# Optimization experiments

Measured on AMD Instinct MI355X. Metric: run time of the kernel, lower is better.

## Reference

```python
import math
import jax, jax.numpy as jnp
import numpy as np

B, T, D = 1, 4096, 1024
NH, NKV, HD = 16, 4, 64          # nhead, n_kv_heads, head_dim
WINDOW = 256


def _alibi_slopes(nhead: int) -> np.ndarray:
    closest_pow2 = 2 ** math.floor(math.log2(nhead))
    base = 2.0 ** (-2.0 ** (-(math.log2(closest_pow2) - 3)))
    slopes = base ** np.arange(1, closest_pow2 + 1, dtype=np.float32)
    if closest_pow2 < nhead:
        extra_base = 2.0 ** (-2.0 ** (-(math.log2(2 * closest_pow2) - 3)))
        extra = extra_base ** np.arange(1, 2 * (nhead - closest_pow2) + 1, 2, dtype=np.float32)
        slopes = np.concatenate([slopes, extra])
    return slopes.astype(np.float32)


def setup_inputs() -> dict:
    key = jax.random.key(0)
    ks = jax.random.split(key, 9)
    s = 0.02
    return {
        "x": jax.random.normal(ks[0], (B, T, D), jnp.float32),
        "Wq": jax.random.normal(ks[1], (D, NH * HD), jnp.float32) * s,
        "bq": jax.random.normal(ks[2], (NH * HD,), jnp.float32) * s,
        "Wk": jax.random.normal(ks[3], (D, NKV * HD), jnp.float32) * s,
        "bk": jax.random.normal(ks[4], (NKV * HD,), jnp.float32) * s,
        "Wv": jax.random.normal(ks[5], (D, NKV * HD), jnp.float32) * s,
        "bv": jax.random.normal(ks[6], (NKV * HD,), jnp.float32) * s,
        "Wo": jax.random.normal(ks[7], (D, D), jnp.float32) * s,
        "bo": jax.random.normal(ks[8], (D,), jnp.float32) * s,
    }


def _attn_bias():
    # ALiBi bias + causal + sliding-window mask, shape (NH, T, T)
    pos = jnp.arange(T)
    dist = pos[None, :] - pos[:, None]          # col - row; <=0 where causal-allowed
    allowed = (dist <= 0) & (-dist < WINDOW)    # causal AND within window
    slopes = jnp.asarray(_alibi_slopes(NH))     # (NH,)
    bias = -slopes[:, None, None] * jnp.abs(dist)[None].astype(jnp.float32)
    return jnp.where(allowed[None], bias, -jnp.inf)  # (NH, T, T)


def reference(x, Wq, bq, Wk, bk, Wv, bv, Wo, bo):
    q = (x @ Wq + bq).reshape(B, T, NH, HD).transpose(0, 2, 1, 3)   # (B,NH,T,HD)
    k = (x @ Wk + bk).reshape(B, T, NKV, HD).transpose(0, 2, 1, 3)  # (B,NKV,T,HD)
    v = (x @ Wv + bv).reshape(B, T, NKV, HD).transpose(0, 2, 1, 3)
    # GQA: repeat_interleave kv heads to NH
    k = jnp.repeat(k, NH // NKV, axis=1)
    v = jnp.repeat(v, NH // NKV, axis=1)
    scale = 1.0 / math.sqrt(HD)
    scores = jnp.einsum("bhtd,bhsd->bhts", q, k) * scale + _attn_bias()[None]
    probs = jax.nn.softmax(scores, axis=-1)
    out = jnp.einsum("bhts,bhsd->bhtd", probs, v)        # (B,NH,T,HD)
    out = out.transpose(0, 2, 1, 3).reshape(B, T, D)
    return out @ Wo + bo
```

## Files before the change

### kernel.cpp

```cpp
#include <hip/hip_runtime.h>

typedef __bf16 bf16;
typedef __bf16 bf16x8 __attribute__((ext_vector_type(8)));
typedef float f32x4 __attribute__((ext_vector_type(4)));

#define T_LEN   4096
#define D_MODEL 1024
#define QKV_LD  1536
#define VT_LD   4128
#define WINDOW  256

__device__ __forceinline__ void gload_lds16(const bf16* g, bf16* l) {
    __builtin_amdgcn_global_load_lds((const __attribute__((address_space(1))) void*)g,
                                     (__attribute__((address_space(3))) void*)l, 16, 0, 0);
}


__global__ void cvt_f32_bf16(const float* __restrict__ in, bf16* __restrict__ out, int n) {
    int i = (blockIdx.x * blockDim.x + threadIdx.x) * 8;
    if (i >= n) return;
    float4 a = *(const float4*)(in + i);
    float4 b = *(const float4*)(in + i + 4);
    bf16x8 o;
    o[0] = (bf16)a.x; o[1] = (bf16)a.y; o[2] = (bf16)a.z; o[3] = (bf16)a.w;
    o[4] = (bf16)b.x; o[5] = (bf16)b.y; o[6] = (bf16)b.z; o[7] = (bf16)b.w;
    *(bf16x8*)(out + i) = o;
}

__global__ void transpose_wqkv(const float* __restrict__ Wq, const float* __restrict__ Wk,
                               const float* __restrict__ Wv, bf16* __restrict__ Wt) {
    __shared__ float t[32][33];
    int n0 = blockIdx.x * 32, k0 = blockIdx.y * 32;
    const float* W; int Ns, nofs;
    if (n0 < 1024)      { W = Wq; Ns = 1024; nofs = 0; }
    else if (n0 < 1280) { W = Wk; Ns = 256;  nofs = 1024; }
    else                { W = Wv; Ns = 256;  nofs = 1280; }
    int tx = threadIdx.x & 31, ty = threadIdx.x >> 5;
#pragma unroll
    for (int it = 0; it < 4; ++it)
        t[ty + it * 8][tx] = W[(size_t)(k0 + ty + it * 8) * Ns + (n0 - nofs) + tx];
    __syncthreads();
#pragma unroll
    for (int it = 0; it < 4; ++it)
        Wt[(size_t)(n0 + ty + it * 8) * 1024 + k0 + tx] = (bf16)t[tx][ty + it * 8];
}

__global__ void transpose_w(const float* __restrict__ W, bf16* __restrict__ Wt, int K, int N) {
    __shared__ float t[32][33];
    int n0 = blockIdx.x * 32, k0 = blockIdx.y * 32;
    int tx = threadIdx.x & 31, ty = threadIdx.x >> 5;
#pragma unroll
    for (int it = 0; it < 4; ++it)
        t[ty + it * 8][tx] = W[(size_t)(k0 + ty + it * 8) * N + n0 + tx];
    __syncthreads();
#pragma unroll
    for (int it = 0; it < 4; ++it)
        Wt[(size_t)(n0 + ty + it * 8) * K + k0 + tx] = (bf16)t[tx][ty + it * 8];
}

__global__ void transpose_v(const bf16* __restrict__ QKV, bf16* __restrict__ Vt) {
    __shared__ bf16 t[32][33];
    int t0 = blockIdx.x * 32;
    int c0 = blockIdx.y * 32;
    int tx = threadIdx.x & 31, ty = threadIdx.x >> 5;
#pragma unroll
    for (int it = 0; it < 4; ++it)
        t[ty + it * 8][tx] = QKV[(size_t)(t0 + ty + it * 8) * QKV_LD + 1280 + c0 + tx];
    __syncthreads();
#pragma unroll
    for (int it = 0; it < 4; ++it)
        Vt[(size_t)(c0 + ty + it * 8) * VT_LD + t0 + tx] = t[tx][ty + it * 8];
}


template <bool OUT_BF16, bool QKV_BIAS>
__global__ __launch_bounds__(256) void gemm_bt(
    const bf16* __restrict__ A, const bf16* __restrict__ Bt,
    const float* __restrict__ b0, const float* __restrict__ b1,
    const float* __restrict__ b2, void* __restrict__ Cv,
    int M, int N, int K)
{
    __shared__ bf16 As[128 * 32];
    __shared__ bf16 Bs[64 * 32];
    const int m0 = blockIdx.y * 128;
    const int n0 = blockIdx.x * 64;
    const int tid  = threadIdx.x;
    const int wave = tid >> 6, lane = tid & 63;
    const int quad = lane >> 4, l16 = lane & 15;
    const int wm = wave >> 1, wn = wave & 1;

    f32x4 acc[4][2] = {};

    const int srow = wave * 16 + (lane >> 2);
    const int scol = (lane & 3) * 8;
    const bf16* ga0 = A  + (size_t)(m0 + srow) * K + scol;
    const bf16* ga1 = A  + (size_t)(m0 + srow + 64) * K + scol;
    const bf16* gb  = Bt + (size_t)(n0 + srow) * K + scol;
    bf16* la0 = As + srow * 32 + scol;
    bf16* la1 = As + (srow + 64) * 32 + scol;
    bf16* lb  = Bs + srow * 32 + scol;

    const int nk = K >> 5;
    for (int kt = 0; kt < nk; ++kt) {
        __syncthreads();
        gload_lds16(ga0 + kt * 32, la0);
        gload_lds16(ga1 + kt * 32, la1);
        gload_lds16(gb  + kt * 32, lb);
        __syncthreads();
        bf16x8 af[4], bfr[2];
#pragma unroll
        for (int i = 0; i < 4; ++i)
            af[i] = *(const bf16x8*)&As[(wm * 64 + i * 16 + l16) * 32 + quad * 8];
#pragma unroll
        for (int j = 0; j < 2; ++j)
            bfr[j] = *(const bf16x8*)&Bs[(wn * 32 + j * 16 + l16) * 32 + quad * 8];
#pragma unroll
        for (int i = 0; i < 4; ++i)
#pragma unroll
            for (int j = 0; j < 2; ++j)
                acc[i][j] = __builtin_amdgcn_mfma_f32_16x16x32_bf16(af[i], bfr[j], acc[i][j], 0, 0, 0);
    }

#pragma unroll
    for (int i = 0; i < 4; ++i)
#pragma unroll
        for (int j = 0; j < 2; ++j) {
            const int col = n0 + wn * 32 + j * 16 + l16;
            const float bb = QKV_BIAS
                ? (col < 1024 ? b0[col] : (col < 1280 ? b1[col - 1024] : b2[col - 1280]))
                : b0[col];
#pragma unroll
            for (int r = 0; r < 4; ++r) {
                const int row = m0 + wm * 64 + i * 16 + quad * 4 + r;
                const float v = acc[i][j][r] + bb;
                if (OUT_BF16) ((bf16*)Cv)[(size_t)row * N + col] = (bf16)v;
                else          ((float*)Cv)[(size_t)row * N + col] = v;
            }
        }
}


__global__ __launch_bounds__(256) void attn_kernel(
    const bf16* __restrict__ QKV, const bf16* __restrict__ Vt, bf16* __restrict__ Oa)
{
    __shared__ bf16 Ps[4][16][296];
    const int wave = threadIdx.x >> 6;
    const int lane = threadIdx.x & 63;
    const int q0 = (blockIdx.x * 4 + wave) * 16;
    const int h  = blockIdx.y;
    const int kh = h >> 2;
    const int quad = lane >> 4, l16 = lane & 15;
    const float slope = exp2f(-0.5f * (float)(h + 1));
    const int lo = (q0 >= 256) ? (q0 - 256) : 0;

    const bf16* qp = QKV + (size_t)(q0 + l16) * QKV_LD + h * 64 + quad * 8;
    bf16x8 qf0 = *(const bf16x8*)qp;
    bf16x8 qf1 = *(const bf16x8*)(qp + 32);

    f32x4 s[17];
#pragma unroll
    for (int t = 0; t < 17; ++t) {
        const bf16* kp = QKV + (size_t)(lo + t * 16 + l16) * QKV_LD + D_MODEL + kh * 64 + quad * 8;
        bf16x8 kf0 = *(const bf16x8*)kp;
        bf16x8 kf1 = *(const bf16x8*)(kp + 32);
        f32x4 a = {};
        a = __builtin_amdgcn_mfma_f32_16x16x32_bf16(qf0, kf0, a, 0, 0, 0);
        a = __builtin_amdgcn_mfma_f32_16x16x32_bf16(qf1, kf1, a, 0, 0, 0);
        s[t] = a;
    }

    float rinv[4];
#pragma unroll
    for (int r = 0; r < 4; ++r) {
        const int row = q0 + quad * 4 + r;
        float mx = -1e30f;
#pragma unroll
        for (int t = 0; t < 17; ++t) {
            const int key = lo + t * 16 + l16;
            float v = s[t][r] * 0.125f - slope * (float)(row - key);
            const bool ok = (key <= row) && (key > row - WINDOW);
            v = ok ? v : -1e30f;
            s[t][r] = v;
            mx = fmaxf(mx, v);
        }
#pragma unroll
        for (int d = 1; d < 16; d <<= 1) mx = fmaxf(mx, __shfl_xor(mx, d));
        float sum = 0.f;
#pragma unroll
        for (int t = 0; t < 17; ++t) {
            float p = __expf(s[t][r] - mx);
            s[t][r] = p;
            sum += p;
        }
#pragma unroll
        for (int d = 1; d < 16; d <<= 1) sum += __shfl_xor(sum, d);
        rinv[r] = 1.f / sum;
    }

    {
        int idx = lane;
#pragma unroll
        for (int it = 0; it < 4; ++it) {
            Ps[wave][(idx >> 4) & 15][272 + (idx & 15)] = (bf16)0.f;
            idx += 64;
        }
    }
#pragma unroll
    for (int t = 0; t < 17; ++t)
#pragma unroll
        for (int r = 0; r < 4; ++r)
            Ps[wave][quad * 4 + r][t * 16 + l16] = (bf16)(s[t][r] * rinv[r]);
    __syncthreads();

    f32x4 o[4] = {};
#pragma unroll
    for (int c = 0; c < 9; ++c) {
        bf16x8 pf = *(const bf16x8*)&Ps[wave][l16][c * 32 + quad * 8];
#pragma unroll
        for (int j = 0; j < 4; ++j) {
            const bf16* vp = Vt + (size_t)(kh * 64 + j * 16 + l16) * VT_LD + lo + c * 32 + quad * 8;
            bf16x8 vf = *(const bf16x8*)vp;
            o[j] = __builtin_amdgcn_mfma_f32_16x16x32_bf16(pf, vf, o[j], 0, 0, 0);
        }
    }

#pragma unroll
    for (int j = 0; j < 4; ++j)
#pragma unroll
        for (int r = 0; r < 4; ++r)
            Oa[(size_t)(q0 + quad * 4 + r) * D_MODEL + h * 64 + j * 16 + l16] = (bf16)o[j][r];
}


extern "C" void kernel_launch(void* const* d_in, const int* in_sizes, int n_in,
                              void* d_out, int out_size, void* d_ws, size_t ws_size,
                              hipStream_t stream) {
    const float* x  = (const float*)d_in[0];
    const float* Wq = (const float*)d_in[1];
    const float* bq = (const float*)d_in[2];
    const float* Wk = (const float*)d_in[3];
    const float* bk = (const float*)d_in[4];
    const float* Wv = (const float*)d_in[5];
    const float* bv = (const float*)d_in[6];
    const float* Wo = (const float*)d_in[7];
    const float* bo = (const float*)d_in[8];
    float* out = (float*)d_out;

    char* ws = (char*)d_ws;
    bf16*  xb    = (bf16*)(ws);
    bf16*  WtQKV = (bf16*)(ws + 8388608);
    bf16*  WtO   = (bf16*)(ws + 11534336);
    bf16*  QKV   = (bf16*)(ws + 13637632);
    bf16*  Vt    = (bf16*)(ws + 26220544);
    bf16*  AO    = (bf16*)(ws + 28334080);

    cvt_f32_bf16<<<2048, 256, 0, stream>>>(x, xb, 4096 * 1024);
    transpose_wqkv<<<dim3(48, 32), 256, 0, stream>>>(Wq, Wk, Wv, WtQKV);
    transpose_w<<<dim3(32, 32), 256, 0, stream>>>(Wo, WtO, 1024, 1024);

    gemm_bt<true, true><<<dim3(24, 32), 256, 0, stream>>>(xb, WtQKV, bq, bk, bv, QKV, 4096, 1536, 1024);
    transpose_v<<<dim3(128, 8), 256, 0, stream>>>(QKV, Vt);
    attn_kernel<<<dim3(64, 16), 256, 0, stream>>>(QKV, Vt, AO);
    gemm_bt<false, false><<<dim3(16, 32), 256, 0, stream>>>(AO, WtO, bo, nullptr, nullptr, out, 4096, 1024, 1024);
}
```

Baseline: 181.2 us.

## Fuse prep kernels, write V transposed from GEMM epilogue, remap blocks per XCD

The three preprocessing kernels (x conversion and both weight transposes) become one launch that dispatches on block index. The transpose_v kernel is removed: the QKV GEMM epilogue writes V tiles straight into the transposed Vt buffer with 4-element vector stores. GEMM blocks are also remapped to a 1D grid so each XCD handles a contiguous band of M rows, aiming for better L2 reuse. Together these cut launch count and one extra pass over V, at the cost of scattered transposed stores in the epilogue.

```diff
diff --git a/kernel.cpp b/kernel.cpp
--- a/kernel.cpp
+++ b/kernel.cpp
@@ -1,6 +1,7 @@
 #include <hip/hip_runtime.h>
 
 typedef __bf16 bf16;
+typedef __bf16 bf16x4 __attribute__((ext_vector_type(4)));
 typedef __bf16 bf16x8 __attribute__((ext_vector_type(8)));
 typedef float f32x4 __attribute__((ext_vector_type(4)));
 
@@ -16,25 +17,37 @@
 }
 
 
-__global__ void cvt_f32_bf16(const float* __restrict__ in, bf16* __restrict__ out, int n) {
-    int i = (blockIdx.x * blockDim.x + threadIdx.x) * 8;
-    if (i >= n) return;
-    float4 a = *(const float4*)(in + i);
-    float4 b = *(const float4*)(in + i + 4);
-    bf16x8 o;
-    o[0] = (bf16)a.x; o[1] = (bf16)a.y; o[2] = (bf16)a.z; o[3] = (bf16)a.w;
-    o[4] = (bf16)b.x; o[5] = (bf16)b.y; o[6] = (bf16)b.z; o[7] = (bf16)b.w;
-    *(bf16x8*)(out + i) = o;
-}
-
-__global__ void transpose_wqkv(const float* __restrict__ Wq, const float* __restrict__ Wk,
-                               const float* __restrict__ Wv, bf16* __restrict__ Wt) {
+__global__ __launch_bounds__(256) void prep_fused(
+    const float* __restrict__ x,
+    const float* __restrict__ Wq, const float* __restrict__ Wk,
+    const float* __restrict__ Wv, const float* __restrict__ Wo,
+    bf16* __restrict__ xb, bf16* __restrict__ WtQKV, bf16* __restrict__ WtO)
+{
     __shared__ float t[32][33];
-    int n0 = blockIdx.x * 32, k0 = blockIdx.y * 32;
-    const float* W; int Ns, nofs;
-    if (n0 < 1024)      { W = Wq; Ns = 1024; nofs = 0; }
-    else if (n0 < 1280) { W = Wk; Ns = 256;  nofs = 1024; }
-    else                { W = Wv; Ns = 256;  nofs = 1280; }
+    const int blk = blockIdx.x;
+    if (blk < 2048) {
+        int i = (blk * 256 + threadIdx.x) * 8;
+        float4 a = *(const float4*)(x + i);
+        float4 b = *(const float4*)(x + i + 4);
+        bf16x8 o;
+        o[0] = (bf16)a.x; o[1] = (bf16)a.y; o[2] = (bf16)a.z; o[3] = (bf16)a.w;
+        o[4] = (bf16)b.x; o[5] = (bf16)b.y; o[6] = (bf16)b.z; o[7] = (bf16)b.w;
+        *(bf16x8*)(xb + i) = o;
+        return;
+    }
+    const float* W; bf16* Wt; int n0, k0, Ns, nofs;
+    if (blk < 3584) {
+        int b = blk - 2048;
+        n0 = (b % 48) * 32; k0 = (b / 48) * 32;
+        if (n0 < 1024)      { W = Wq; Ns = 1024; nofs = 0; }
+        else if (n0 < 1280) { W = Wk; Ns = 256;  nofs = 1024; }
+        else                { W = Wv; Ns = 256;  nofs = 1280; }
+        Wt = WtQKV;
+    } else {
+        int b = blk - 3584;
+        n0 = (b % 32) * 32; k0 = (b / 32) * 32;
+        W = Wo; Ns = 1024; nofs = 0; Wt = WtO;
+    }
     int tx = threadIdx.x & 31, ty = threadIdx.x >> 5;
 #pragma unroll
     for (int it = 0; it < 4; ++it)
@@ -43,33 +56,6 @@
 #pragma unroll
     for (int it = 0; it < 4; ++it)
         Wt[(size_t)(n0 + ty + it * 8) * 1024 + k0 + tx] = (bf16)t[tx][ty + it * 8];
-}
-
-__global__ void transpose_w(const float* __restrict__ W, bf16* __restrict__ Wt, int K, int N) {
-    __shared__ float t[32][33];
-    int n0 = blockIdx.x * 32, k0 = blockIdx.y * 32;
-    int tx = threadIdx.x & 31, ty = threadIdx.x >> 5;
-#pragma unroll
-    for (int it = 0; it < 4; ++it)
-        t[ty + it * 8][tx] = W[(size_t)(k0 + ty + it * 8) * N + n0 + tx];
-    __syncthreads();
-#pragma unroll
-    for (int it = 0; it < 4; ++it)
-        Wt[(size_t)(n0 + ty + it * 8) * K + k0 + tx] = (bf16)t[tx][ty + it * 8];
-}
-
-__global__ void transpose_v(const bf16* __restrict__ QKV, bf16* __restrict__ Vt) {
-    __shared__ bf16 t[32][33];
-    int t0 = blockIdx.x * 32;
-    int c0 = blockIdx.y * 32;
-    int tx = threadIdx.x & 31, ty = threadIdx.x >> 5;
-#pragma unroll
-    for (int it = 0; it < 4; ++it)
-        t[ty + it * 8][tx] = QKV[(size_t)(t0 + ty + it * 8) * QKV_LD + 1280 + c0 + tx];
-    __syncthreads();
-#pragma unroll
-    for (int it = 0; it < 4; ++it)
-        Vt[(size_t)(c0 + ty + it * 8) * VT_LD + t0 + tx] = t[tx][ty + it * 8];
 }
 
 
@@ -77,13 +63,16 @@
 __global__ __launch_bounds__(256) void gemm_bt(
     const bf16* __restrict__ A, const bf16* __restrict__ Bt,
     const float* __restrict__ b0, const float* __restrict__ b1,
-    const float* __restrict__ b2, void* __restrict__ Cv,
-    int M, int N, int K)
+    const float* __restrict__ b2, void* __restrict__ Cv, bf16* __restrict__ Vt,
+    int M, int N, int K, int nbx, int bands_per_xcd)
 {
     __shared__ bf16 As[128 * 32];
     __shared__ bf16 Bs[64 * 32];
-    const int m0 = blockIdx.y * 128;
-    const int n0 = blockIdx.x * 64;
+    const int blk = blockIdx.x;
+    const int xcd = blk & 7;
+    const int s   = blk >> 3;
+    const int m0 = (xcd * bands_per_xcd + s / nbx) * 128;
+    const int n0 = (s % nbx) * 64;
     const int tid  = threadIdx.x;
     const int wave = tid >> 6, lane = tid & 63;
     const int quad = lane >> 4, l16 = lane & 15;
@@ -121,6 +110,7 @@
                 acc[i][j] = __builtin_amdgcn_mfma_f32_16x16x32_bf16(af[i], bfr[j], acc[i][j], 0, 0, 0);
     }
 
+    const bool vtile = QKV_BIAS && (n0 >= 1280);
 #pragma unroll
     for (int i = 0; i < 4; ++i)
 #pragma unroll
@@ -129,12 +119,19 @@
             const float bb = QKV_BIAS
                 ? (col < 1024 ? b0[col] : (col < 1280 ? b1[col - 1024] : b2[col - 1280]))
                 : b0[col];
-#pragma unroll
-            for (int r = 0; r < 4; ++r) {
-                const int row = m0 + wm * 64 + i * 16 + quad * 4 + r;
-                const float v = acc[i][j][r] + bb;
-                if (OUT_BF16) ((bf16*)Cv)[(size_t)row * N + col] = (bf16)v;
-                else          ((float*)Cv)[(size_t)row * N + col] = v;
+            const int row0 = m0 + wm * 64 + i * 16 + quad * 4;
+            if (vtile) {
+                bf16x4 pv;
+#pragma unroll
+                for (int r = 0; r < 4; ++r) pv[r] = (bf16)(acc[i][j][r] + bb);
+                *(bf16x4*)&Vt[(size_t)(col - 1280) * VT_LD + row0] = pv;
+            } else {
+#pragma unroll
+                for (int r = 0; r < 4; ++r) {
+                    const float v = acc[i][j][r] + bb;
+                    if (OUT_BF16) ((bf16*)Cv)[(size_t)(row0 + r) * N + col] = (bf16)v;
+                    else          ((float*)Cv)[(size_t)(row0 + r) * N + col] = v;
+                }
             }
         }
 }
@@ -254,12 +251,13 @@
     bf16*  Vt    = (bf16*)(ws + 26220544);
     bf16*  AO    = (bf16*)(ws + 28334080);
 
-    cvt_f32_bf16<<<2048, 256, 0, stream>>>(x, xb, 4096 * 1024);
-    transpose_wqkv<<<dim3(48, 32), 256, 0, stream>>>(Wq, Wk, Wv, WtQKV);
-    transpose_w<<<dim3(32, 32), 256, 0, stream>>>(Wo, WtO, 1024, 1024);
-
-    gemm_bt<true, true><<<dim3(24, 32), 256, 0, stream>>>(xb, WtQKV, bq, bk, bv, QKV, 4096, 1536, 1024);
-    transpose_v<<<dim3(128, 8), 256, 0, stream>>>(QKV, Vt);
+    prep_fused<<<4608, 256, 0, stream>>>(x, Wq, Wk, Wv, Wo, xb, WtQKV, WtO);
+
+    gemm_bt<true, true><<<768, 256, 0, stream>>>(
+        xb, WtQKV, bq, bk, bv, QKV, Vt, 4096, 1536, 1024, 24, 4);
+
     attn_kernel<<<dim3(64, 16), 256, 0, stream>>>(QKV, Vt, AO);
-    gemm_bt<false, false><<<dim3(16, 32), 256, 0, stream>>>(AO, WtO, bo, nullptr, nullptr, out, 4096, 1024, 1024);
-}
+
+    gemm_bt<false, false><<<512, 256, 0, stream>>>(
+        AO, WtO, bo, nullptr, nullptr, out, nullptr, 4096, 1024, 1024, 16, 4);
+}
```

After: 172.9 us. 1.05x faster.
